# Kernel optimization log

Hardware: AMD Instinct MI355X
Metric: run time of the kernel (lower is better)

The kernel has to match this reference:

```python
import jax, jax.numpy as jnp
import numpy as np

FEAT_DIM = 16
NUM_DEPTHS = 64


def _lookat(p):
    z = p / np.linalg.norm(p)
    up = np.array([0.0, 1.0, 0.0])
    x = np.cross(up, z); x = x / np.linalg.norm(x)
    y = np.cross(z, x)
    m = np.eye(4)
    m[:3, 0] = x; m[:3, 1] = y; m[:3, 2] = z; m[:3, 3] = p
    return m


def setup_inputs() -> dict:
    key = jax.random.key(0)
    ks = jax.random.split(key, 6)
    S, Vin, Vt, C, D, H, W = 2, 3, 4, FEAT_DIM, NUM_DEPTHS, 96, 96
    enc = jax.random.normal(ks[0], (S, Vin, C, D, H, W), jnp.float32) * 0.5
    rng = np.random.default_rng(0)

    def poses(n):
        ps = rng.normal(size=(S, n, 3))
        ps = ps / np.linalg.norm(ps, axis=-1, keepdims=True) * 1.3
        return jnp.asarray(np.stack([[_lookat(ps[i, j]) for j in range(n)] for i in range(S)]), jnp.float32)

    input_poses = poses(Vin)
    target_poses = poses(Vt)
    W1 = jax.random.normal(ks[1], (16, 64), jnp.float32) * 0.25
    W2 = jax.random.normal(ks[2], (64, 64), jnp.float32) * 0.125
    W3 = jax.random.normal(ks[3], (64, 17), jnp.float32) * 0.125
    return dict(
        encoded_imgs=enc, input_poses=input_poses, target_poses=target_poses,
        focal=1.2, z_near=0.8, z_far=1.8, samples_per_ray=64,
        W1=W1, b1=jnp.zeros((64,), jnp.float32),
        W2=W2, b2=jnp.zeros((64,), jnp.float32),
        W3=W3, b3=jnp.zeros((17,), jnp.float32),
    )


def grid_sample_3d(vol, grid):
    # vol: (N,C,D,H,W); grid: (N,P,3) xyz in [-1,1]; trilinear, zero padding, align_corners=False
    N, C, D, H, W = vol.shape
    P = grid.shape[1]
    ix = ((grid[..., 0] + 1.0) * W - 1.0) * 0.5
    iy = ((grid[..., 1] + 1.0) * H - 1.0) * 0.5
    iz = ((grid[..., 2] + 1.0) * D - 1.0) * 0.5
    x0, y0, z0 = jnp.floor(ix), jnp.floor(iy), jnp.floor(iz)
    volf = vol.reshape(N, C, D * H * W)
    out = jnp.zeros((N, C, P), vol.dtype)
    for dz in (0, 1):
        for dy in (0, 1):
            for dx in (0, 1):
                xc, yc, zc = x0 + dx, y0 + dy, z0 + dz
                wgt = (1.0 - jnp.abs(ix - xc)) * (1.0 - jnp.abs(iy - yc)) * (1.0 - jnp.abs(iz - zc))
                valid = ((xc >= 0) & (xc < W) & (yc >= 0) & (yc < H) & (zc >= 0) & (zc < D))
                xi = jnp.clip(xc, 0, W - 1).astype(jnp.int32)
                yi = jnp.clip(yc, 0, H - 1).astype(jnp.int32)
                zi = jnp.clip(zc, 0, D - 1).astype(jnp.int32)
                idx = (zi * H + yi) * W + xi  # (N,P)
                vals = jnp.take_along_axis(volf, idx[:, None, :], axis=2)  # (N,C,P)
                out = out + (wgt * valid)[:, None, :] * vals
    return out


def _upsample2_align_corners(x):
    # bilinear x2 on last two axes, align_corners=True (torch UpsamplingBilinear2d)
    def interp(x, axis):
        n = x.shape[axis]
        m = 2 * n
        pos = jnp.arange(m) * ((n - 1) / (m - 1))
        lo = jnp.floor(pos).astype(jnp.int32)
        hi = jnp.minimum(lo + 1, n - 1)
        f = (pos - lo).astype(x.dtype)
        xl = jnp.take(x, lo, axis=axis)
        xh = jnp.take(x, hi, axis=axis)
        shp = [1] * x.ndim; shp[axis] = m
        f = f.reshape(shp)
        return xl * (1.0 - f) + xh * f
    return interp(interp(x, -2), -1)


def _forward(encoded_imgs, input_poses, target_poses, focal, z_near, z_far,
             samples_per_ray, W1, b1, W2, b2, W3, b3):
    S, Vin, C, D, H, W = encoded_imgs.shape
    Vt = target_poses.shape[1]
    h, w = H // 2, W // 2
    spr = samples_per_ray
    dt = encoded_imgs.dtype

    # --- gen_rays at half resolution ---
    poses = target_poses.reshape(S * Vt, 4, 4)
    ys = ((jnp.arange(h, dtype=dt) + 0.5) / h) * 2.0 - 1.0
    xs = ((jnp.arange(w, dtype=dt) + 0.5) / w) * 2.0 - 1.0
    yy, xx = jnp.meshgrid(ys, xs, indexing='ij')
    dirs_cam = jnp.stack([xx / focal, -yy / focal, -jnp.ones_like(xx)], -1)  # (h,w,3)
    dirs = jnp.einsum('bij,hwj->bhwi', poses[:, :3, :3], dirs_cam)            # (B,h,w,3)
    origins = poses[:, None, None, :3, 3]                                      # (B,1,1,3)

    t = z_near + (z_far - z_near) * (jnp.arange(spr, dtype=dt) / (spr - 1))
    times = jnp.broadcast_to(t, (S * Vt, h, w, spr))
    pts = origins[..., None, :] + times[..., None] * dirs[..., None, :]        # (B,h,w,spr,3)

    times = times.reshape(S, Vt, h, w, spr)
    pts = pts.reshape(S, Vt, h, w, spr, 3)
    pts_h = jnp.concatenate([pts, jnp.ones_like(pts[..., :1])], axis=-1)      # (S,Vt,h,w,spr,4)

    # --- invert input poses (rigid) ---
    R = input_poses[..., :3, :3]
    tr = input_poses[..., :3, 3]
    Rt = jnp.swapaxes(R, -1, -2)
    inv_t = -jnp.einsum('svij,svj->svi', Rt, tr)
    top = jnp.concatenate([Rt, inv_t[..., None]], axis=-1)                     # (S,Vin,3,4)
    bottom = jnp.broadcast_to(jnp.array([0.0, 0.0, 0.0, 1.0], dt), (S, Vin, 1, 4))
    extrinsics = jnp.concatenate([top, bottom], axis=-2)                       # (S,Vin,4,4)

    local = jnp.einsum('svij,sthwpj->svthwpi', extrinsics, pts_h)              # (S,Vin,Vt,h,w,spr,4)
    x = local[..., 0]
    y = local[..., 1]
    z = -local[..., 2]
    u = x / z * focal
    v = y / z * focal
    min_z, max_z = focal * z_near, focal * z_far
    wd = 2.0 * (z - min_z) / (max_z - min_z) - 1.0
    uvw = jnp.stack((u, -v, -wd), axis=-1)                                     # (S,Vin,Vt,h,w,spr,3)

    feats = grid_sample_3d(encoded_imgs.reshape(S * Vin, C, D, H, W),
                           uvw.reshape(S * Vin, -1, 3))                        # (S*Vin,C,P)
    feats = feats.reshape(S, Vin, C, Vt, h, w, spr)
    feats = jnp.mean(feats, axis=1)                                            # baseline_mean camera weighting
    feats = jnp.transpose(feats, (0, 2, 3, 4, 5, 1))                           # (S,Vt,h,w,spr,C)

    # --- MLP with residual feature skip ---
    x1 = jax.nn.relu(feats @ W1 + b1)
    x2 = jax.nn.relu(x1 @ W2 + b2)
    out = x2 @ W3 + b3                                                         # (...,17)
    density = jax.nn.relu(out[..., 0])
    rgb = feats + out[..., 1:]

    # --- volume rendering ---
    deltas = times[..., 1:] - times[..., :-1]
    last = jnp.full_like(deltas[..., :1], 1e10)
    deltas = jnp.concatenate([deltas, last], axis=-1)
    sigdel = density * deltas
    alpha = 1.0 - jnp.exp(-sigdel)
    transmittance = jnp.exp(-jnp.cumsum(sigdel, axis=-1))
    wts = alpha * transmittance
    renders = jnp.sum(wts[..., None] * rgb, axis=-2)                           # (S,Vt,h,w,16)

    renders = jnp.transpose(renders, (0, 1, 4, 2, 3))                          # (S,Vt,16,h,w)
    renders = _upsample2_align_corners(renders.reshape(S * Vt, C, h, w))
    return renders.reshape(S, Vt, C, H, W)


def reference(encoded_imgs, input_poses, target_poses, focal, z_near, z_far,
              samples_per_ray, W1, b1, W2, b2, W3, b3):
    return _forward(encoded_imgs, input_poses, target_poses, float(focal), float(z_near),
                    float(z_far), int(samples_per_ray), W1, b1, W2, b2, W3, b3)
```

## Files before the change

kernel.cpp:

```cpp
#include <hip/hip_runtime.h>
#include <hip/hip_bf16.h>
#include <math.h>

#define NS   2
#define NVIN 3
#define NVT  4
#define NC   16
#define ND   64
#define NH   96
#define NW   96
#define HWH  48
#define SPR  64
#define DHW  (ND*NH*NW)
#define NTILE (DHW / 64)
#define NSAMP (NS*NVT*HWH*HWH*SPR)
#define NRAYS (NS*NVT*HWH*HWH)

typedef __attribute__((ext_vector_type(8))) short bfrag;
typedef __attribute__((ext_vector_type(4))) float cfrag;

#define MFMA16 __builtin_amdgcn_mfma_f32_16x16x32_bf16

#define WAVE_LDS_SYNC() asm volatile("s_waitcnt lgkmcnt(0)" ::: "memory")

__device__ __forceinline__ short f2bf(float x) {
    union { __hip_bfloat16 b; short s; } cv;
    cv.b = __float2bfloat16(x);
    return cv.s;
}
__device__ __forceinline__ float bf2f(short s) {
    union { unsigned int u; float f; } cv;
    cv.u = ((unsigned int)(unsigned short)s) << 16;
    return cv.f;
}

__device__ __forceinline__ void mk_frag(const float* p, bfrag& ah, bfrag& al) {
    float4 v0 = *(const float4*)p;
    float4 v1 = *(const float4*)(p + 4);
    float e[8] = {v0.x, v0.y, v0.z, v0.w, v1.x, v1.y, v1.z, v1.w};
    #pragma unroll
    for (int j = 0; j < 8; j++) {
        short h = f2bf(e[j]);
        ah[j] = h;
        al[j] = f2bf(e[j] - bf2f(h));
    }
}

__global__ __launch_bounds__(256) void wprep_kernel(
    const float* __restrict__ W1, const float* __restrict__ W2,
    const float* __restrict__ W3, short* __restrict__ whi, short* __restrict__ wlo)
{
    int t = blockIdx.x * 256 + threadIdx.x;
    int f = t >> 6, L = t & 63;
    int q = L >> 4, li = L & 15;
    #pragma unroll
    for (int j = 0; j < 8; j++) {
        int kloc = q * 8 + j;
        float w = 0.f;
        if (f < 4) {
            int n = f * 16 + li, k = kloc;
            if (k < 16) w = W1[k * 64 + n];
        } else if (f < 12) {
            int kt = (f - 4) >> 2, nt = (f - 4) & 3;
            w = W2[(kt * 32 + kloc) * 64 + nt * 16 + li];
        } else {
            int kt = (f - 12) >> 1, nt = (f - 12) & 1;
            int n = nt * 16 + li;
            if (n < 17) w = W3[(kt * 32 + kloc) * 17 + n];
        }
        short h = f2bf(w);
        whi[(f * 64 + L) * 8 + j] = h;
        wlo[(f * 64 + L) * 8 + j] = f2bf(w - bf2f(h));
    }
}

__global__ __launch_bounds__(256) void transpose_kernel(
    const float* __restrict__ in, float* __restrict__ out)
{
    __shared__ float tile[NC][64 + 4];
    const int t   = threadIdx.x;
    const int blk = blockIdx.x;
    const int vox0 = (blk % NTILE) * 64;
    const int sv   = blk / NTILE;

    const int c  = t >> 4;
    const int vg = (t & 15) * 4;
    const float* src = in + ((size_t)sv * NC + c) * DHW + vox0 + vg;
    float4 v = *(const float4*)src;
    tile[c][vg + 0] = v.x; tile[c][vg + 1] = v.y;
    tile[c][vg + 2] = v.z; tile[c][vg + 3] = v.w;
    __syncthreads();

    const int ov = t >> 2;
    const int oc = (t & 3) * 4;
    float4 w = make_float4(tile[oc + 0][ov], tile[oc + 1][ov],
                           tile[oc + 2][ov], tile[oc + 3][ov]);
    float* dst = out + ((size_t)sv * DHW + vox0 + ov) * NC + oc;
    *(float4*)dst = w;
}

__global__ __launch_bounds__(256) void gather_kernel(
    const float* __restrict__ enc_t,
    const float* __restrict__ ipose,
    const float* __restrict__ tpose,
    const float* __restrict__ focal_p,
    const float* __restrict__ znear_p,
    const float* __restrict__ zfar_p,
    float* __restrict__ xbuf)
{
    const int ray = (blockIdx.x & 7) * (NRAYS >> 3) + (blockIdx.x >> 3);
    const int c4  = threadIdx.x & 3;
    const int d   = threadIdx.x >> 2;
    const int px  = ray % HWH;
    const int py  = (ray / HWH) % HWH;
    const int b   = ray / (HWH * HWH);
    const int s   = b >> 2;

    const float focal = focal_p[0];
    const float znear = znear_p[0];
    const float zfar  = zfar_p[0];

    const float* P = tpose + b * 16;
    float ysc = ((py + 0.5f) / (float)HWH) * 2.f - 1.f;
    float xsc = ((px + 0.5f) / (float)HWH) * 2.f - 1.f;
    float dcx = xsc / focal, dcy = -ysc / focal, dcz = -1.f;
    float dirx = P[0]*dcx + P[1]*dcy + P[2]*dcz;
    float diry = P[4]*dcx + P[5]*dcy + P[6]*dcz;
    float dirz = P[8]*dcx + P[9]*dcy + P[10]*dcz;

    float tv  = znear + (zfar - znear) * ((float)d / (float)(SPR - 1));
    float ptx = P[3] + tv * dirx, pty = P[7] + tv * diry, ptz = P[11] + tv * dirz;

    const float minz = focal * znear, maxz = focal * zfar;
    float f0 = 0.f, f1 = 0.f, f2 = 0.f, f3 = 0.f;

    #pragma unroll
    for (int v = 0; v < NVIN; v++) {
        const float* E = ipose + (s * NVIN + v) * 16;
        float qx = ptx - E[3], qy = pty - E[7], qz = ptz - E[11];
        float lx = E[0]*qx + E[4]*qy + E[8]*qz;
        float ly = E[1]*qx + E[5]*qy + E[9]*qz;
        float lz = E[2]*qx + E[6]*qy + E[10]*qz;
        float zz = -lz;
        float u  = lx / zz * focal;
        float vv = ly / zz * focal;
        float wd = 2.f * (zz - minz) / (maxz - minz) - 1.f;
        float ix = ((u   + 1.f) * NW - 1.f) * 0.5f;
        float iy = ((-vv + 1.f) * NH - 1.f) * 0.5f;
        float iz = ((-wd + 1.f) * ND - 1.f) * 0.5f;
        float x0 = floorf(ix), y0 = floorf(iy), z0 = floorf(iz);
        float x1 = x0 + 1.f,   y1 = y0 + 1.f,   z1 = z0 + 1.f;

        float wxa0 = 1.f - fabsf(ix - x0), wxa1 = 1.f - fabsf(ix - x1);
        float wya0 = 1.f - fabsf(iy - y0), wya1 = 1.f - fabsf(iy - y1);
        float wza0 = 1.f - fabsf(iz - z0), wza1 = 1.f - fabsf(iz - z1);
        wxa0 = (x0 >= 0.f && x0 < (float)NW) ? wxa0 : 0.f;
        wxa1 = (x1 >= 0.f && x1 < (float)NW) ? wxa1 : 0.f;
        wya0 = (y0 >= 0.f && y0 < (float)NH) ? wya0 : 0.f;
        wya1 = (y1 >= 0.f && y1 < (float)NH) ? wya1 : 0.f;
        wza0 = (z0 >= 0.f && z0 < (float)ND) ? wza0 : 0.f;
        wza1 = (z1 >= 0.f && z1 < (float)ND) ? wza1 : 0.f;
        int xi0 = min(max((int)x0, 0), NW - 1), xi1 = min(max((int)x1, 0), NW - 1);
        int yi0 = min(max((int)y0, 0), NH - 1), yi1 = min(max((int)y1, 0), NH - 1);
        int zi0 = min(max((int)z0, 0), ND - 1), zi1 = min(max((int)z1, 0), ND - 1);
        int o00 = (zi0 * NH + yi0) * NW, o01 = (zi0 * NH + yi1) * NW;
        int o10 = (zi1 * NH + yi0) * NW, o11 = (zi1 * NH + yi1) * NW;

        const float wxv[2] = {wxa0, wxa1};
        const float wyv[2] = {wya0, wya1};
        const float wzv[2] = {wza0, wza1};
        const int   xiv[2] = {xi0, xi1};
        const int   ozy[2][2] = {{o00, o01}, {o10, o11}};

        const float* VB = enc_t + (size_t)(s * NVIN + v) * DHW * NC;
        #pragma unroll
        for (int k = 0; k < 8; k++) {
            const int dx = k & 1, dy = (k >> 1) & 1, dz = k >> 2;
            float w = (wxv[dx] * wyv[dy]) * wzv[dz];
            int idx = ozy[dz][dy] + xiv[dx];
            float4 a = *(const float4*)(VB + (size_t)idx * NC + c4 * 4);
            f0 += w * a.x; f1 += w * a.y; f2 += w * a.z; f3 += w * a.w;
        }
    }
    const float inv3 = 1.f / 3.f;
    ((float4*)xbuf)[(ray * 64 + d) * 4 + c4] =
        make_float4(f0 * inv3, f1 * inv3, f2 * inv3, f3 * inv3);
}

__global__ __launch_bounds__(256) void mlp_kernel(
    const float* __restrict__ xbuf,
    const float* __restrict__ znear_p,
    const float* __restrict__ zfar_p,
    const short* __restrict__ whi, const short* __restrict__ wlo,
    const float* __restrict__ B1, const float* __restrict__ B2,
    const float* __restrict__ B3,
    float* __restrict__ rhalf)
{
    const int lane = threadIdx.x & 63;
    const int ray  = blockIdx.x * 4 + (threadIdx.x >> 6);
    const int px   = ray % HWH;
    const int py   = (ray / HWH) % HWH;
    const int b    = ray / (HWH * HWH);

    const float znear = znear_p[0];
    const float zfar  = zfar_p[0];

    __shared__ float sbuf[4][64][36];
    float (*B)[36] = sbuf[threadIdx.x >> 6];
    const int li = lane & 15, q = lane >> 4;
    const float* X = xbuf + (size_t)ray * 64 * NC;

    float b1v[4], b2v[4], b3v[2];
    #pragma unroll
    for (int nt = 0; nt < 4; nt++) { b1v[nt] = B1[nt*16 + li]; b2v[nt] = B2[nt*16 + li]; }
    b3v[0] = B3[li];
    b3v[1] = (li == 0) ? B3[16] : 0.f;

    bfrag xah[4], xal[4];
    bfrag zb = {0,0,0,0,0,0,0,0};
    #pragma unroll
    for (int mt = 0; mt < 4; mt++) {
        if (q < 2) mk_frag(X + (mt*16 + li) * NC + q * 8, xah[mt], xal[mt]);
        else { xah[mt] = zb; xal[mt] = zb; }
    }

    cfrag zc = {0.f, 0.f, 0.f, 0.f};
    cfrag h2acc[4][4];
    #pragma unroll
    for (int mt = 0; mt < 4; mt++)
        #pragma unroll
        for (int nt = 0; nt < 4; nt++) h2acc[mt][nt] = zc;

    #pragma unroll
    for (int c1 = 0; c1 < 2; c1++) {
        cfrag h1[4][2];
        #pragma unroll
        for (int nt2 = 0; nt2 < 2; nt2++) {
            int f = 2*c1 + nt2;
            bfrag bh = *(const bfrag*)(whi + (f*64 + lane)*8);
            bfrag bl = *(const bfrag*)(wlo + (f*64 + lane)*8);
            #pragma unroll
            for (int mt = 0; mt < 4; mt++) {
                cfrag a = zc;
                a = MFMA16(xal[mt], bh, a, 0, 0, 0);
                a = MFMA16(xah[mt], bl, a, 0, 0, 0);
                a = MFMA16(xah[mt], bh, a, 0, 0, 0);
                h1[mt][nt2] = a;
            }
        }
        WAVE_LDS_SYNC();
        #pragma unroll
        for (int mt = 0; mt < 4; mt++)
            #pragma unroll
            for (int nt2 = 0; nt2 < 2; nt2++)
                #pragma unroll
                for (int r = 0; r < 4; r++)
                    B[mt*16 + q*4 + r][nt2*16 + li] =
                        fmaxf(h1[mt][nt2][r] + b1v[2*c1 + nt2], 0.f);
        WAVE_LDS_SYNC();
        bfrag hah[4], hal[4];
        #pragma unroll
        for (int mt = 0; mt < 4; mt++)
            mk_frag(&B[mt*16 + li][q*8], hah[mt], hal[mt]);
        #pragma unroll
        for (int nt = 0; nt < 4; nt++) {
            int f = 4 + c1*4 + nt;
            bfrag bh = *(const bfrag*)(whi + (f*64 + lane)*8);
            bfrag bl = *(const bfrag*)(wlo + (f*64 + lane)*8);
            #pragma unroll
            for (int mt = 0; mt < 4; mt++) {
                cfrag a = h2acc[mt][nt];
                a = MFMA16(hal[mt], bh, a, 0, 0, 0);
                a = MFMA16(hah[mt], bl, a, 0, 0, 0);
                a = MFMA16(hah[mt], bh, a, 0, 0, 0);
                h2acc[mt][nt] = a;
            }
        }
    }

    cfrag oacc[4][2];
    #pragma unroll
    for (int mt = 0; mt < 4; mt++)
        #pragma unroll
        for (int nt = 0; nt < 2; nt++) oacc[mt][nt] = zc;

    #pragma unroll
    for (int c2 = 0; c2 < 2; c2++) {
        WAVE_LDS_SYNC();
        #pragma unroll
        for (int mt = 0; mt < 4; mt++)
            #pragma unroll
            for (int nt2 = 0; nt2 < 2; nt2++)
                #pragma unroll
                for (int r = 0; r < 4; r++)
                    B[mt*16 + q*4 + r][nt2*16 + li] =
                        fmaxf(h2acc[mt][2*c2 + nt2][r] + b2v[2*c2 + nt2], 0.f);
        WAVE_LDS_SYNC();
        bfrag hah[4], hal[4];
        #pragma unroll
        for (int mt = 0; mt < 4; mt++)
            mk_frag(&B[mt*16 + li][q*8], hah[mt], hal[mt]);
        #pragma unroll
        for (int nt = 0; nt < 2; nt++) {
            int f = 12 + c2*2 + nt;
            bfrag bh = *(const bfrag*)(whi + (f*64 + lane)*8);
            bfrag bl = *(const bfrag*)(wlo + (f*64 + lane)*8);
            #pragma unroll
            for (int mt = 0; mt < 4; mt++) {
                cfrag a = oacc[mt][nt];
                a = MFMA16(hal[mt], bh, a, 0, 0, 0);
                a = MFMA16(hah[mt], bl, a, 0, 0, 0);
                a = MFMA16(hah[mt], bh, a, 0, 0, 0);
                oacc[mt][nt] = a;
            }
        }
    }

    WAVE_LDS_SYNC();
    #pragma unroll
    for (int mt = 0; mt < 4; mt++)
        #pragma unroll
        for (int nt = 0; nt < 2; nt++) {
            int ch = nt*16 + li;
            if (ch < 17) {
                #pragma unroll
                for (int r = 0; r < 4; r++)
                    B[mt*16 + q*4 + r][ch] = oacc[mt][nt][r] + b3v[nt];
            }
        }
    WAVE_LDS_SYNC();
    float4 o0 = *(float4*)&B[lane][0];
    float4 o1 = *(float4*)&B[lane][4];
    float4 o2 = *(float4*)&B[lane][8];
    float4 o3 = *(float4*)&B[lane][12];
    float o16 = B[lane][16];

    float density = fmaxf(o0.x, 0.f);
    float orgb[16] = {o0.y, o0.z, o0.w, o1.x, o1.y, o1.z, o1.w, o2.x,
                      o2.y, o2.z, o2.w, o3.x, o3.y, o3.z, o3.w, o16};

    float4 fx0 = *(const float4*)(X + lane * NC + 0);
    float4 fx1 = *(const float4*)(X + lane * NC + 4);
    float4 fx2 = *(const float4*)(X + lane * NC + 8);
    float4 fx3 = *(const float4*)(X + lane * NC + 12);
    float feats[16] = {fx0.x, fx0.y, fx0.z, fx0.w, fx1.x, fx1.y, fx1.z, fx1.w,
                       fx2.x, fx2.y, fx2.z, fx2.w, fx3.x, fx3.y, fx3.z, fx3.w};

    float tv = znear + (zfar - znear) * ((float)lane / (float)(SPR - 1));
    float tn = znear + (zfar - znear) * ((float)(lane + 1) / (float)(SPR - 1));
    float delta = (lane < SPR - 1) ? (tn - tv) : 1e10f;
    float sigdel = density * delta;
    float alpha = 1.f - expf(-sigdel);
    float csum = sigdel;
    #pragma unroll
    for (int off = 1; off < 64; off <<= 1) {
        float nb = __shfl_up(csum, off, 64);
        if (lane >= off) csum += nb;
    }
    float wray = alpha * expf(-csum);

    #pragma unroll
    for (int c = 0; c < NC; c++) {
        float val = wray * (feats[c] + orgb[c]);
        #pragma unroll
        for (int off = 32; off >= 1; off >>= 1)
            val += __shfl_down(val, off, 64);
        if (lane == 0)
            rhalf[((b * NC + c) * HWH + py) * HWH + px] = val;
    }
}

__device__ __forceinline__ void mlp_and_composite(
    const float feats[NC], int lane, int b, int py, int px,
    float tv, float znear, float zfar,
    const float* __restrict__ W1, const float* __restrict__ B1,
    const float* __restrict__ W2, const float* __restrict__ B2,
    const float* __restrict__ W3, const float* __restrict__ B3,
    float* __restrict__ rhalf)
{
    float outa[17];
    #pragma unroll
    for (int c = 0; c < 17; c++) outa[c] = B3[c];
    for (int kc = 0; kc < 4; kc++) {
        float h2c[16];
        #pragma unroll
        for (int k = 0; k < 16; k++) h2c[k] = B2[kc * 16 + k];
        #pragma unroll 4
        for (int j = 0; j < 64; j++) {
            float a = B1[j];
            #pragma unroll
            for (int i = 0; i < NC; i++) a += feats[i] * W1[i * 64 + j];
            a = fmaxf(a, 0.f);
            const float* w2p = W2 + j * 64 + kc * 16;
            #pragma unroll
            for (int k = 0; k < 16; k++) h2c[k] += a * w2p[k];
        }
        #pragma unroll
        for (int k = 0; k < 16; k++) {
            float hv = fmaxf(h2c[k], 0.f);
            const float* w3p = W3 + (kc * 16 + k) * 17;
            #pragma unroll
            for (int c = 0; c < 17; c++) outa[c] += hv * w3p[c];
        }
    }
    float density = fmaxf(outa[0], 0.f);
    float tn = znear + (zfar - znear) * ((float)(lane + 1) / (float)(SPR - 1));
    float delta = (lane < SPR - 1) ? (tn - tv) : 1e10f;
    float sigdel = density * delta;
    float alpha = 1.f - expf(-sigdel);
    float csum = sigdel;
    #pragma unroll
    for (int off = 1; off < 64; off <<= 1) {
        float nb = __shfl_up(csum, off, 64);
        if (lane >= off) csum += nb;
    }
    float wray = alpha * expf(-csum);
    #pragma unroll
    for (int c = 0; c < NC; c++) {
        float val = wray * (feats[c] + outa[1 + c]);
        #pragma unroll
        for (int off = 32; off >= 1; off >>= 1)
            val += __shfl_down(val, off, 64);
        if (lane == 0)
            rhalf[((b * NC + c) * HWH + py) * HWH + px] = val;
    }
}

__global__ __launch_bounds__(256) void render_kernel(
    const float* __restrict__ enc,
    const float* __restrict__ ipose,
    const float* __restrict__ tpose,
    const float* __restrict__ focal_p,
    const float* __restrict__ znear_p,
    const float* __restrict__ zfar_p,
    const float* __restrict__ W1, const float* __restrict__ B1,
    const float* __restrict__ W2, const float* __restrict__ B2,
    const float* __restrict__ W3, const float* __restrict__ B3,
    float* __restrict__ rhalf)
{
    const int lane = threadIdx.x & 63;
    const int ray  = blockIdx.x * 4 + (threadIdx.x >> 6);
    const int px   = ray % HWH;
    const int py   = (ray / HWH) % HWH;
    const int b    = ray / (HWH * HWH);
    const int s    = b >> 2;
    const float focal = focal_p[0];
    const float znear = znear_p[0];
    const float zfar  = zfar_p[0];
    const float* P = tpose + b * 16;
    float ysc = ((py + 0.5f) / (float)HWH) * 2.f - 1.f;
    float xsc = ((px + 0.5f) / (float)HWH) * 2.f - 1.f;
    float dcx = xsc / focal, dcy = -ysc / focal, dcz = -1.f;
    float dirx = P[0]*dcx + P[1]*dcy + P[2]*dcz;
    float diry = P[4]*dcx + P[5]*dcy + P[6]*dcz;
    float dirz = P[8]*dcx + P[9]*dcy + P[10]*dcz;
    float tv  = znear + (zfar - znear) * ((float)lane / (float)(SPR - 1));
    float ptx = P[3] + tv * dirx, pty = P[7] + tv * diry, ptz = P[11] + tv * dirz;
    float feats[NC];
    #pragma unroll
    for (int c = 0; c < NC; c++) feats[c] = 0.f;
    const float minz = focal * znear, maxz = focal * zfar;
    for (int v = 0; v < NVIN; v++) {
        const float* E = ipose + (s * NVIN + v) * 16;
        float qx = ptx - E[3], qy = pty - E[7], qz = ptz - E[11];
        float lx = E[0]*qx + E[4]*qy + E[8]*qz;
        float ly = E[1]*qx + E[5]*qy + E[9]*qz;
        float lz = E[2]*qx + E[6]*qy + E[10]*qz;
        float zz = -lz;
        float u  = lx / zz * focal;
        float vv = ly / zz * focal;
        float wd = 2.f * (zz - minz) / (maxz - minz) - 1.f;
        float ix = ((u   + 1.f) * NW - 1.f) * 0.5f;
        float iy = ((-vv + 1.f) * NH - 1.f) * 0.5f;
        float iz = ((-wd + 1.f) * ND - 1.f) * 0.5f;
        float x0 = floorf(ix), y0 = floorf(iy), z0 = floorf(iz);
        float wgt[8]; int idx[8];
        #pragma unroll
        for (int k = 0; k < 8; k++) {
            float xc = x0 + (k & 1), yc = y0 + ((k >> 1) & 1), zc = z0 + (k >> 2);
            float wt = (1.f - fabsf(ix - xc)) * (1.f - fabsf(iy - yc)) * (1.f - fabsf(iz - zc));
            bool valid = (xc >= 0.f) && (xc < (float)NW) &&
                         (yc >= 0.f) && (yc < (float)NH) &&
                         (zc >= 0.f) && (zc < (float)ND);
            wgt[k] = valid ? wt : 0.f;
            int xi = min(max((int)xc, 0), NW - 1);
            int yi = min(max((int)yc, 0), NH - 1);
            int zi = min(max((int)zc, 0), ND - 1);
            idx[k] = (zi * NH + yi) * NW + xi;
        }
        const float* VB = enc + (size_t)(s * NVIN + v) * NC * DHW;
        #pragma unroll
        for (int c = 0; c < NC; c++) {
            const float* vc = VB + c * DHW;
            float acc = 0.f;
            #pragma unroll
            for (int k = 0; k < 8; k++) acc += wgt[k] * vc[idx[k]];
            feats[c] += acc;
        }
    }
    #pragma unroll
    for (int c = 0; c < NC; c++) feats[c] *= (1.f / 3.f);
    mlp_and_composite(feats, lane, b, py, px, tv, znear, zfar,
                      W1, B1, W2, B2, W3, B3, rhalf);
}

__global__ __launch_bounds__(256) void upsample_kernel(
    const float* __restrict__ in, float* __restrict__ out)
{
    int tid = blockIdx.x * 256 + threadIdx.x;
    int ox = tid % NW;
    int oy = (tid / NW) % NH;
    int c  = (tid / (NW * NH)) % NC;
    int b  = tid / (NW * NH * NC);
    const float sc = (float)((HWH - 1) / (double)(NH - 1));
    float pyf = oy * sc;
    float pxf = ox * sc;
    int y0 = (int)floorf(pyf); int y1 = min(y0 + 1, HWH - 1); float fy = pyf - y0;
    int x0 = (int)floorf(pxf); int x1 = min(x0 + 1, HWH - 1); float fx = pxf - x0;
    const float* src = in + (b * NC + c) * HWH * HWH;
    float v00 = src[y0 * HWH + x0], v01 = src[y0 * HWH + x1];
    float v10 = src[y1 * HWH + x0], v11 = src[y1 * HWH + x1];
    float gl = v00 * (1.f - fy) + v10 * fy;
    float gr = v01 * (1.f - fy) + v11 * fy;
    out[tid] = gl * (1.f - fx) + gr * fx;
}

extern "C" void kernel_launch(void* const* d_in, const int* in_sizes, int n_in,
                              void* d_out, int out_size, void* d_ws, size_t ws_size,
                              hipStream_t stream) {
    const float* enc   = (const float*)d_in[0];
    const float* ipose = (const float*)d_in[1];
    const float* tpose = (const float*)d_in[2];
    const float* focal = (const float*)d_in[3];
    const float* znear = (const float*)d_in[4];
    const float* zfar  = (const float*)d_in[5];
    const float* W1 = (const float*)d_in[7];
    const float* B1 = (const float*)d_in[8];
    const float* W2 = (const float*)d_in[9];
    const float* B2 = (const float*)d_in[10];
    const float* W3 = (const float*)d_in[11];
    const float* B3 = (const float*)d_in[12];

    float* out = (float*)d_out;
    const int nrays = NRAYS;
    const int nout  = NS * NVT * NC * NH * NW;
    const size_t enc_t_bytes = (size_t)NS * NVIN * NC * DHW * 4;
    const size_t rhalf_bytes = (size_t)nrays * NC * 4;
    const size_t wfrag_bytes = 16 * 64 * 8 * sizeof(short);
    const size_t xbuf_bytes  = (size_t)NSAMP * NC * 4;

    if (ws_size >= enc_t_bytes + rhalf_bytes + 2 * wfrag_bytes + xbuf_bytes) {
        char* base = (char*)d_ws;
        float* enc_t = (float*)base;                      base += enc_t_bytes;
        float* rhalf = (float*)base;                      base += rhalf_bytes;
        short* whi   = (short*)base;                      base += wfrag_bytes;
        short* wlo   = (short*)base;                      base += wfrag_bytes;
        float* xbuf  = (float*)base;

        wprep_kernel<<<4, 256, 0, stream>>>(W1, W2, W3, whi, wlo);
        transpose_kernel<<<NS * NVIN * NTILE, 256, 0, stream>>>(enc, enc_t);
        gather_kernel<<<nrays, 256, 0, stream>>>(
            enc_t, ipose, tpose, focal, znear, zfar, xbuf);
        mlp_kernel<<<nrays / 4, 256, 0, stream>>>(
            xbuf, znear, zfar, whi, wlo, B1, B2, B3, rhalf);
        upsample_kernel<<<nout / 256, 256, 0, stream>>>(rhalf, out);
    } else {
        float* rhalf = (float*)d_ws;
        render_kernel<<<nrays / 4, 256, 0, stream>>>(
            enc, ipose, tpose, focal, znear, zfar,
            W1, B1, W2, B2, W3, B3, rhalf);
        upsample_kernel<<<nout / 256, 256, 0, stream>>>(rhalf, out);
    }
}
```

Before: 616.7 us.

## Split trilinear x-corners across lanes and batch gather loads per sample

Result: no change. 607.4 us (-1.5%).

```diff
diff --git a/kernel.cpp b/kernel.cpp
--- a/kernel.cpp
+++ b/kernel.cpp
@@ -108,13 +108,16 @@
     const float* __restrict__ zfar_p,
     float* __restrict__ xbuf)
 {
-    const int ray = (blockIdx.x & 7) * (NRAYS >> 3) + (blockIdx.x >> 3);
-    const int c4  = threadIdx.x & 3;
-    const int d   = threadIdx.x >> 2;
-    const int px  = ray % HWH;
-    const int py  = (ray / HWH) % HWH;
-    const int b   = ray / (HWH * HWH);
-    const int s   = b >> 2;
+    const int ray  = (blockIdx.x & 7) * (NRAYS >> 3) + (blockIdx.x >> 3);
+    const int lane = threadIdx.x & 63;
+    const int wv   = threadIdx.x >> 6;
+    const int c4   = lane & 3;
+    const int xbit = (lane >> 2) & 1;
+    const int ds   = lane >> 3;
+    const int px   = ray % HWH;
+    const int py   = (ray / HWH) % HWH;
+    const int b    = ray / (HWH * HWH);
+    const int s    = b >> 2;
 
     const float focal = focal_p[0];
     const float znear = znear_p[0];
@@ -128,63 +131,92 @@
     float diry = P[4]*dcx + P[5]*dcy + P[6]*dcz;
     float dirz = P[8]*dcx + P[9]*dcy + P[10]*dcz;
 
-    float tv  = znear + (zfar - znear) * ((float)d / (float)(SPR - 1));
-    float ptx = P[3] + tv * dirx, pty = P[7] + tv * diry, ptz = P[11] + tv * dirz;
-
-    const float minz = focal * znear, maxz = focal * zfar;
-    float f0 = 0.f, f1 = 0.f, f2 = 0.f, f3 = 0.f;
-
+    float lox[NVIN], loy[NVIN], loz[NVIN];
+    float ldx[NVIN], ldy[NVIN], ldz[NVIN];
     #pragma unroll
     for (int v = 0; v < NVIN; v++) {
         const float* E = ipose + (s * NVIN + v) * 16;
-        float qx = ptx - E[3], qy = pty - E[7], qz = ptz - E[11];
-        float lx = E[0]*qx + E[4]*qy + E[8]*qz;
-        float ly = E[1]*qx + E[5]*qy + E[9]*qz;
-        float lz = E[2]*qx + E[6]*qy + E[10]*qz;
-        float zz = -lz;
-        float u  = lx / zz * focal;
-        float vv = ly / zz * focal;
-        float wd = 2.f * (zz - minz) / (maxz - minz) - 1.f;
-        float ix = ((u   + 1.f) * NW - 1.f) * 0.5f;
-        float iy = ((-vv + 1.f) * NH - 1.f) * 0.5f;
-        float iz = ((-wd + 1.f) * ND - 1.f) * 0.5f;
-        float x0 = floorf(ix), y0 = floorf(iy), z0 = floorf(iz);
-        float x1 = x0 + 1.f,   y1 = y0 + 1.f,   z1 = z0 + 1.f;
-
-        float wxa0 = 1.f - fabsf(ix - x0), wxa1 = 1.f - fabsf(ix - x1);
-        float wya0 = 1.f - fabsf(iy - y0), wya1 = 1.f - fabsf(iy - y1);
-        float wza0 = 1.f - fabsf(iz - z0), wza1 = 1.f - fabsf(iz - z1);
-        wxa0 = (x0 >= 0.f && x0 < (float)NW) ? wxa0 : 0.f;
-        wxa1 = (x1 >= 0.f && x1 < (float)NW) ? wxa1 : 0.f;
-        wya0 = (y0 >= 0.f && y0 < (float)NH) ? wya0 : 0.f;
-        wya1 = (y1 >= 0.f && y1 < (float)NH) ? wya1 : 0.f;
-        wza0 = (z0 >= 0.f && z0 < (float)ND) ? wza0 : 0.f;
-        wza1 = (z1 >= 0.f && z1 < (float)ND) ? wza1 : 0.f;
-        int xi0 = min(max((int)x0, 0), NW - 1), xi1 = min(max((int)x1, 0), NW - 1);
-        int yi0 = min(max((int)y0, 0), NH - 1), yi1 = min(max((int)y1, 0), NH - 1);
-        int zi0 = min(max((int)z0, 0), ND - 1), zi1 = min(max((int)z1, 0), ND - 1);
-        int o00 = (zi0 * NH + yi0) * NW, o01 = (zi0 * NH + yi1) * NW;
-        int o10 = (zi1 * NH + yi0) * NW, o11 = (zi1 * NH + yi1) * NW;
-
-        const float wxv[2] = {wxa0, wxa1};
-        const float wyv[2] = {wya0, wya1};
-        const float wzv[2] = {wza0, wza1};
-        const int   xiv[2] = {xi0, xi1};
-        const int   ozy[2][2] = {{o00, o01}, {o10, o11}};
-
-        const float* VB = enc_t + (size_t)(s * NVIN + v) * DHW * NC;
-        #pragma unroll
-        for (int k = 0; k < 8; k++) {
-            const int dx = k & 1, dy = (k >> 1) & 1, dz = k >> 2;
-            float w = (wxv[dx] * wyv[dy]) * wzv[dz];
-            int idx = ozy[dz][dy] + xiv[dx];
-            float4 a = *(const float4*)(VB + (size_t)idx * NC + c4 * 4);
-            f0 += w * a.x; f1 += w * a.y; f2 += w * a.z; f3 += w * a.w;
-        }
-    }
+        float qx = P[3] - E[3], qy = P[7] - E[7], qz = P[11] - E[11];
+        lox[v] = E[0]*qx + E[4]*qy + E[8]*qz;
+        loy[v] = E[1]*qx + E[5]*qy + E[9]*qz;
+        loz[v] = E[2]*qx + E[6]*qy + E[10]*qz;
+        ldx[v] = E[0]*dirx + E[4]*diry + E[8]*dirz;
+        ldy[v] = E[1]*dirx + E[5]*diry + E[9]*dirz;
+        ldz[v] = E[2]*dirx + E[6]*diry + E[10]*dirz;
+    }
+
+    const float minz = focal * znear, maxz = focal * zfar;
     const float inv3 = 1.f / 3.f;
-    ((float4*)xbuf)[(ray * 64 + d) * 4 + c4] =
-        make_float4(f0 * inv3, f1 * inv3, f2 * inv3, f3 * inv3);
+
+    #pragma unroll 1
+    for (int iter = 0; iter < 2; iter++) {
+        const int d = wv * 8 + ds + iter * 32;
+        float tv = znear + (zfar - znear) * ((float)d / (float)(SPR - 1));
+
+        float wgt[12];
+        int   off[12];
+        #pragma unroll
+        for (int v = 0; v < NVIN; v++) {
+            float lx = lox[v] + tv * ldx[v];
+            float ly = loy[v] + tv * ldy[v];
+            float lz = loz[v] + tv * ldz[v];
+            float zz = -lz;
+            float u  = lx / zz * focal;
+            float vv = ly / zz * focal;
+            float wd = 2.f * (zz - minz) / (maxz - minz) - 1.f;
+            float ix = ((u   + 1.f) * NW - 1.f) * 0.5f;
+            float iy = ((-vv + 1.f) * NH - 1.f) * 0.5f;
+            float iz = ((-wd + 1.f) * ND - 1.f) * 0.5f;
+            float x0 = floorf(ix), y0 = floorf(iy), z0 = floorf(iz);
+            float x1 = x0 + 1.f,   y1 = y0 + 1.f,   z1 = z0 + 1.f;
+
+            float wxa0 = 1.f - fabsf(ix - x0), wxa1 = 1.f - fabsf(ix - x1);
+            float wya0 = 1.f - fabsf(iy - y0), wya1 = 1.f - fabsf(iy - y1);
+            float wza0 = 1.f - fabsf(iz - z0), wza1 = 1.f - fabsf(iz - z1);
+            wxa0 = (x0 >= 0.f && x0 < (float)NW) ? wxa0 : 0.f;
+            wxa1 = (x1 >= 0.f && x1 < (float)NW) ? wxa1 : 0.f;
+            wya0 = (y0 >= 0.f && y0 < (float)NH) ? wya0 : 0.f;
+            wya1 = (y1 >= 0.f && y1 < (float)NH) ? wya1 : 0.f;
+            wza0 = (z0 >= 0.f && z0 < (float)ND) ? wza0 : 0.f;
+            wza1 = (z1 >= 0.f && z1 < (float)ND) ? wza1 : 0.f;
+
+            int xi0 = min(max((int)x0, 0), NW - 1), xi1 = min(max((int)x1, 0), NW - 1);
+            int yi0 = min(max((int)y0, 0), NH - 1), yi1 = min(max((int)y1, 0), NH - 1);
+            int zi0 = min(max((int)z0, 0), ND - 1), zi1 = min(max((int)z1, 0), ND - 1);
+            int o00 = (zi0 * NH + yi0) * NW, o01 = (zi0 * NH + yi1) * NW;
+            int o10 = (zi1 * NH + yi0) * NW, o11 = (zi1 * NH + yi1) * NW;
+
+            float wxl = xbit ? wxa1 : wxa0;
+            int   xil = xbit ? xi1  : xi0;
+
+            wgt[v*4 + 0] = (wxl * wya0) * wza0;  off[v*4 + 0] = (o00 + xil) * NC + c4 * 4;
+            wgt[v*4 + 1] = (wxl * wya1) * wza0;  off[v*4 + 1] = (o01 + xil) * NC + c4 * 4;
+            wgt[v*4 + 2] = (wxl * wya0) * wza1;  off[v*4 + 2] = (o10 + xil) * NC + c4 * 4;
+            wgt[v*4 + 3] = (wxl * wya1) * wza1;  off[v*4 + 3] = (o11 + xil) * NC + c4 * 4;
+        }
+
+        float4 av[12];
+        #pragma unroll
+        for (int j = 0; j < 12; j++) {
+            const float* VB = enc_t + (size_t)(s * NVIN + (j >> 2)) * DHW * NC;
+            av[j] = *(const float4*)(VB + off[j]);
+        }
+
+        float f0 = 0.f, f1 = 0.f, f2 = 0.f, f3 = 0.f;
+        #pragma unroll
+        for (int j = 0; j < 12; j++) {
+            f0 += wgt[j] * av[j].x; f1 += wgt[j] * av[j].y;
+            f2 += wgt[j] * av[j].z; f3 += wgt[j] * av[j].w;
+        }
+        f0 += __shfl_xor(f0, 4, 64);
+        f1 += __shfl_xor(f1, 4, 64);
+        f2 += __shfl_xor(f2, 4, 64);
+        f3 += __shfl_xor(f3, 4, 64);
+
+        if (!xbit)
+            ((float4*)xbuf)[(ray * 64 + d) * 4 + c4] =
+                make_float4(f0 * inv3, f1 * inv3, f2 * inv3, f3 * inv3);
+    }
 }
 
 __global__ __launch_bounds__(256) void mlp_kernel(
```
